# Optimization experiments

Hardware: AMD Instinct MI355X
Metric: run time of the kernel (lower is better)

## Reference

```python
import jax, jax.numpy as jnp
import numpy as np

D = 1024
H = 16
DK = D // H


def setup_inputs() -> dict:
    key = jax.random.key(0)
    ks = jax.random.split(key, 10)
    B, S = 2, 2048
    scale = 1.0 / np.sqrt(D)
    inp = {
        "x": jax.random.normal(ks[0], (B, S, D), dtype=jnp.float32),
        "mask": jax.random.randint(ks[1], (B, S), 0, 2, dtype=jnp.int32),
        "wq": jax.random.normal(ks[2], (D, D), dtype=jnp.float32) * scale,
        "bq": jnp.zeros((D,), dtype=jnp.float32),
        "wk": jax.random.normal(ks[3], (D, D), dtype=jnp.float32) * scale,
        "bk": jnp.zeros((D,), dtype=jnp.float32),
        "wv": jax.random.normal(ks[4], (D, D), dtype=jnp.float32) * scale,
        "bv": jnp.zeros((D,), dtype=jnp.float32),
        "wo": jax.random.normal(ks[5], (D, D), dtype=jnp.float32) * scale,
        "bo": jnp.zeros((D,), dtype=jnp.float32),
    }
    return inp


def reference(x, mask, wq, bq, wk, bk, wv, bv, wo, bo):
    B, S, _ = x.shape
    # torch Linear: y = x @ W.T + b
    def proj(w, b):
        return (jnp.einsum("bsd,ed->bse", x, w) + b).reshape(B, S, H, DK).transpose(0, 2, 1, 3)  # (B,H,S,dk)

    q = proj(wq, bq)
    k = proj(wk, bk)
    v = proj(wv, bv)

    scores = jnp.einsum("bhqd,bhkd->bhqk", q, k) / jnp.sqrt(jnp.float32(DK))  # (B,H,S,S)
    # original: mask.unsqueeze(1).unsqueeze(3) -> (B,1,S,1), masks along the QUERY axis
    m = mask[:, None, :, None]  # (B,1,S,1)
    scores = jnp.where(m == 0, jnp.float32(-1e9), scores)
    attn = jax.nn.softmax(scores, axis=-1)
    ctx = jnp.einsum("bhqk,bhkd->bhqd", attn, v)  # (B,H,S,dk)
    concat = ctx.transpose(0, 2, 1, 3).reshape(B, S, D)
    return jnp.einsum("bsd,ed->bse", concat, wo) + bo
```

## Files before the change

### kernel.cpp

```cpp
#include <hip/hip_runtime.h>
#include <hip/hip_bf16.h>

#define SEQ 2048
#define DM  1024

typedef __attribute__((ext_vector_type(8))) _Float16 f16x8;
typedef __attribute__((ext_vector_type(4)))  float   f32x4;

#define EXP2F(x) __builtin_amdgcn_exp2f(x)

__device__ __forceinline__ ushort f2h(float x) {
    union { _Float16 h; ushort u; } c; c.h = (_Float16)x; return c.u;
}
__device__ __forceinline__ unsigned pk2h(float a, float b) {
    typedef __fp16 fp16v2 __attribute__((ext_vector_type(2)));
    union { fp16v2 h; unsigned u; } c;
    c.h = __builtin_amdgcn_cvt_pkrtz(a, b);
    return c.u;
}

__device__ __forceinline__ void gload16(const void* g, void* l) {
    __builtin_amdgcn_global_load_lds(
        (const __attribute__((address_space(1))) unsigned*)(uintptr_t)g,
        (__attribute__((address_space(3))) unsigned*)(uintptr_t)l, 16, 0, 0);
}

__global__ __launch_bounds__(256)
void cvt_all(const float* __restrict__ x,  const float* __restrict__ wq,
             const float* __restrict__ wk, const float* __restrict__ wv,
             const float* __restrict__ wo,
             ushort* __restrict__ xH, ushort* __restrict__ wH)
{
    const int NX4 = (2 * SEQ * DM) / 4;
    const int NW4 = (DM * DM) / 4;
    const int total = NX4 + 4 * NW4;
    for (int i = blockIdx.x * 256 + threadIdx.x; i < total; i += gridDim.x * 256) {
        float4 v; ushort4* dst;
        if (i < NX4) {
            v = ((const float4*)x)[i];
            dst = (ushort4*)xH + i;
        } else {
            const int j = i - NX4;
            const int wi = j >> 18;
            const int jo = j & (NW4 - 1);
            const float* ws_ = (wi == 0) ? wq : (wi == 1) ? wk : (wi == 2) ? wv : wo;
            v = ((const float4*)ws_)[jo];
            dst = (ushort4*)wH + j;
        }
        ushort4 h;
        h.x = f2h(v.x); h.y = f2h(v.y); h.z = f2h(v.z); h.w = f2h(v.w);
        *dst = h;
    }
}

template<int BM, int BN, int WM, int WN, int MODE>
__global__ __launch_bounds__(WM * WN * 64)
void gemm5(const ushort* __restrict__ A, const ushort* __restrict__ B,
           const float* __restrict__ b0, const float* __restrict__ b1,
           const float* __restrict__ b2,
           ushort* __restrict__ QH, ushort* __restrict__ KH,
           ushort* __restrict__ VH, float* __restrict__ outf, int nmt)
{
    constexpr int NW  = WM * WN;
    constexpr int PR  = BM / WM, PC = BN / WN;
    constexpr int MR  = PR / 16, NR = PC / 16, MH = MR / 2;
    constexpr int APW = (BM / 8) / NW;
    constexpr int BPW = (BN / 8) / NW;
    constexpr int NT  = DM / 64;

    __shared__ ushort A_lds[2][BM * 64];
    __shared__ ushort B_lds[2][BN * 64];

    const int tid = threadIdx.x, w = tid >> 6, lane = tid & 63;
    const int nwg = gridDim.x, q8 = nwg >> 3;
    const int wg  = (blockIdx.x & 7) * q8 + (blockIdx.x >> 3);
    const int m0  = (wg % nmt) * BM, n0 = (wg / nmt) * BN;
    const int wm  = w / WN, wn = w % WN;

    auto stage = [&](int buf, int kt) {
        const int k0 = kt * 64;
#pragma unroll
        for (int j = 0; j < APW; ++j) {
            const int s   = w * APW + j;
            const int row = s * 8 + (lane >> 3);
            const int cl  = (lane & 7) ^ (row & 7);
            gload16(A + (size_t)(m0 + row) * DM + k0 + cl * 8,
                    &A_lds[buf][s * 512]);
        }
#pragma unroll
        for (int j = 0; j < BPW; ++j) {
            const int s   = w * BPW + j;
            const int row = s * 8 + (lane >> 3);
            const int cl  = (lane & 7) ^ (row & 7);
            gload16(B + (size_t)(n0 + row) * DM + k0 + cl * 8,
                    &B_lds[buf][s * 512]);
        }
    };

    f32x4 acc[MR][NR];
#pragma unroll
    for (int i = 0; i < MR; ++i)
#pragma unroll
        for (int j = 0; j < NR; ++j) acc[i][j] = f32x4{0.f, 0.f, 0.f, 0.f};

    stage(0, 0);
    stage(1, 1);

    for (int t = 0; t < NT; ++t) {
        const int buf = t & 1;
        if (t == NT - 1) asm volatile("s_waitcnt vmcnt(0)" ::: "memory");
        else             asm volatile("s_waitcnt vmcnt(8)" ::: "memory");
        __builtin_amdgcn_sched_barrier(0);
        __builtin_amdgcn_s_barrier();

        f16x8 bf_[NR][2];
#pragma unroll
        for (int nf = 0; nf < NR; ++nf) {
            const int r = wn * PC + nf * 16 + (lane & 15);
#pragma unroll
            for (int kb = 0; kb < 2; ++kb) {
                const int c = kb * 4 + (lane >> 4);
                bf_[nf][kb] = *(const f16x8*)&B_lds[buf][r * 64 + ((c ^ (r & 7)) << 3)];
            }
        }
#pragma unroll
        for (int qm = 0; qm < 2; ++qm) {
            f16x8 af_[MH][2];
#pragma unroll
            for (int mf = 0; mf < MH; ++mf) {
                const int r = wm * PR + qm * (PR / 2) + mf * 16 + (lane & 15);
#pragma unroll
                for (int kb = 0; kb < 2; ++kb) {
                    const int c = kb * 4 + (lane >> 4);
                    af_[mf][kb] = *(const f16x8*)&A_lds[buf][r * 64 + ((c ^ (r & 7)) << 3)];
                }
            }
            __builtin_amdgcn_s_setprio(1);
#pragma unroll
            for (int kb = 0; kb < 2; ++kb)
#pragma unroll
                for (int mf = 0; mf < MH; ++mf)
#pragma unroll
                    for (int nf = 0; nf < NR; ++nf)
                        acc[qm * MH + mf][nf] = __builtin_amdgcn_mfma_f32_16x16x32_f16(
                            af_[mf][kb], bf_[nf][kb], acc[qm * MH + mf][nf], 0, 0, 0);
            __builtin_amdgcn_s_setprio(0);
        }
        __builtin_amdgcn_sched_barrier(0);
        __builtin_amdgcn_s_barrier();
        __builtin_amdgcn_sched_barrier(0);
        if (t + 2 < NT) stage(buf, t + 2);
    }

#pragma unroll
    for (int mf = 0; mf < MR; ++mf)
#pragma unroll
        for (int nf = 0; nf < NR; ++nf) {
            const int col  = n0 + wn * PC + nf * 16 + (lane & 15);
            const int row0 = m0 + wm * PR + mf * 16 + ((lane >> 4) << 2);
            f32x4 v = acc[mf][nf];
            if constexpr (MODE == 1) {
                float4 o;
                o.x = v[0] + b0[row0 + 0];
                o.y = v[1] + b0[row0 + 1];
                o.z = v[2] + b0[row0 + 2];
                o.w = v[3] + b0[row0 + 3];
                *(float4*)&outf[(size_t)col * DM + row0] = o;
            } else {
                const int sel = row0 >> 10;
                const int e = row0 & 1023;
                const int b = col >> 11, s = col & 2047;
                const int h = e >> 6, dk = e & 63;
                const float* bp = (sel == 0) ? b0 : (sel == 1) ? b1 : b2;
                const float sc = (sel == 0) ? 0.125f * 1.44269504089f : 1.0f;
                const float v0 = (v[0] + bp[e + 0]) * sc;
                const float v1 = (v[1] + bp[e + 1]) * sc;
                const float v2 = (v[2] + bp[e + 2]) * sc;
                const float v3 = (v[3] + bp[e + 3]) * sc;
                const int bh = b * 16 + h;
                ushort4 hv;
                hv.x = f2h(v0); hv.y = f2h(v1); hv.z = f2h(v2); hv.w = f2h(v3);
                if (sel == 0) {
                    const size_t off = ((size_t)bh * SEQ + s) * 64 + dk;
                    *(ushort4*)&QH[off] = hv;
                } else if (sel == 1) {
                    const size_t off = ((size_t)bh * SEQ + s) * 64 + dk;
                    *(ushort4*)&KH[off] = hv;
                } else {
                    const size_t o0 = ((size_t)bh * 64 + dk) * SEQ + s;
                    VH[o0]           = hv.x;
                    VH[o0 + SEQ]     = hv.y;
                    VH[o0 + 2 * SEQ] = hv.z;
                    VH[o0 + 3 * SEQ] = hv.w;
                }
            }
        }
}

__global__ __launch_bounds__(512, 2)
void attn_k(const ushort* __restrict__ QH, const ushort* __restrict__ KH,
            const ushort* __restrict__ VH, const int* __restrict__ mask,
            ushort* __restrict__ ch)
{
    __shared__ ushort Ks[4][64 * 64];
    __shared__ ushort Vs[4][64 * 64];
    __shared__ ushort Ps[8][16 * 64];

    const int t = threadIdx.x, w = t >> 6, lane = t & 63;
    const int wg = (blockIdx.x & 7) * 64 + (blockIdx.x >> 3);
    const int bh = wg >> 4, qt = wg & 15;
    const int b = bh >> 4, h = bh & 15;
    const int q0 = qt * 128 + w * 16;
    const size_t base = (size_t)bh * SEQ * 64;
    const int lq = lane & 15, cb = lane >> 4;

    const int msk = mask[b * SEQ + q0 + lq];
    f16x8 qf[2];
#pragma unroll
    for (int kb = 0; kb < 2; ++kb) {
        qf[kb] = *(const f16x8*)&QH[base + (size_t)(q0 + lq) * 64 + kb * 32 + cb * 8];
        if (msk == 0) qf[kb] = f16x8{0, 0, 0, 0, 0, 0, 0, 0};
    }

    float l_part = 0.f;
    f32x4 acc[4];
#pragma unroll
    for (int df = 0; df < 4; ++df) acc[df] = f32x4{0.f, 0.f, 0.f, 0.f};

    const int srow = w * 8 + (lane >> 3);
    const int scl  = (lane & 7) ^ (srow & 7);
    const ushort* gK = &KH[base + (size_t)srow * 64 + scl * 8];
    const ushort* gV = &VH[base + (size_t)srow * SEQ + scl * 8];
    const int wbase = w * 512;
    auto issue_pair = [&](const int B0, const int B1) {
        gload16(gK, &Ks[B0][wbase]); gK += 4096;
        gload16(gV, &Vs[B0][wbase]); gV += 64;
        gload16(gK, &Ks[B1][wbase]); gK += 4096;
        gload16(gV, &Vs[B1][wbase]); gV += 64;
    };

    issue_pair(0, 1);
    issue_pair(2, 3);

    auto compute = [&](const int BUF) {
        f32x4 st[4];
#pragma unroll
        for (int mf = 0; mf < 4; ++mf) st[mf] = f32x4{0.f, 0.f, 0.f, 0.f};
        __builtin_amdgcn_s_setprio(1);
#pragma unroll
        for (int mf = 0; mf < 4; ++mf) {
            const int r = mf * 16 + lq;
#pragma unroll
            for (int kb = 0; kb < 2; ++kb) {
                const int p = (kb * 4 + cb) ^ (r & 7);
                f16x8 kf = *(const f16x8*)&Ks[BUF][r * 64 + p * 8];
                st[mf] = __builtin_amdgcn_mfma_f32_16x16x32_f16(kf, qf[kb], st[mf], 0, 0, 0);
            }
        }
        __builtin_amdgcn_s_setprio(0);

#pragma unroll
        for (int mf = 0; mf < 2; ++mf) {
            const float e0 = EXP2F(st[mf][0]);
            const float e1 = EXP2F(st[mf][1]);
            const float e2 = EXP2F(st[mf][2]);
            const float e3 = EXP2F(st[mf][3]);
            l_part += (e0 + e1) + (e2 + e3);
            uint2 pw;
            pw.x = pk2h(e0, e1);
            pw.y = pk2h(e2, e3);
            const int key0 = mf * 16 + (cb << 2);
            const int p = (key0 >> 3) ^ (lq & 7);
            *(uint2*)&Ps[w][lq * 64 + p * 8 + (key0 & 7)] = pw;
        }
        {
            const int p0 = cb ^ (lq & 7);
            f16x8 pf0 = *(const f16x8*)&Ps[w][lq * 64 + p0 * 8];
            __builtin_amdgcn_s_setprio(1);
#pragma unroll
            for (int df = 0; df < 4; ++df) {
                const int r = df * 16 + lq;
                const int p = cb ^ (r & 7);
                f16x8 vf = *(const f16x8*)&Vs[BUF][r * 64 + p * 8];
                acc[df] = __builtin_amdgcn_mfma_f32_16x16x32_f16(vf, pf0, acc[df], 0, 0, 0);
            }
            __builtin_amdgcn_s_setprio(0);
        }
#pragma unroll
        for (int mf = 2; mf < 4; ++mf) {
            const float e0 = EXP2F(st[mf][0]);
            const float e1 = EXP2F(st[mf][1]);
            const float e2 = EXP2F(st[mf][2]);
            const float e3 = EXP2F(st[mf][3]);
            l_part += (e0 + e1) + (e2 + e3);
            uint2 pw;
            pw.x = pk2h(e0, e1);
            pw.y = pk2h(e2, e3);
            const int key0 = mf * 16 + (cb << 2);
            const int p = (key0 >> 3) ^ (lq & 7);
            *(uint2*)&Ps[w][lq * 64 + p * 8 + (key0 & 7)] = pw;
        }
        {
            const int p1 = (4 + cb) ^ (lq & 7);
            f16x8 pf1 = *(const f16x8*)&Ps[w][lq * 64 + p1 * 8];
            __builtin_amdgcn_s_setprio(1);
#pragma unroll
            for (int df = 0; df < 4; ++df) {
                const int r = df * 16 + lq;
                const int p = (4 + cb) ^ (r & 7);
                f16x8 vf = *(const f16x8*)&Vs[BUF][r * 64 + p * 8];
                acc[df] = __builtin_amdgcn_mfma_f32_16x16x32_f16(vf, pf1, acc[df], 0, 0, 0);
            }
            __builtin_amdgcn_s_setprio(0);
        }
    };

    auto step = [&](const int PH, const bool ISSUE, const bool LAST) {
        if (LAST) asm volatile("s_waitcnt vmcnt(0)" ::: "memory");
        else      asm volatile("s_waitcnt vmcnt(4)" ::: "memory");
        __builtin_amdgcn_sched_barrier(0);
        __builtin_amdgcn_s_barrier();
        compute(PH ? 2 : 0);
        compute(PH ? 3 : 1);
        if (ISSUE) {
            __builtin_amdgcn_sched_barrier(0);
            asm volatile("s_waitcnt lgkmcnt(0)" ::: "memory");
            __builtin_amdgcn_s_barrier();
            __builtin_amdgcn_sched_barrier(0);
            if (PH) issue_pair(2, 3); else issue_pair(0, 1);
        }
    };

#pragma unroll 1
    for (int i = 0; i < 7; ++i) {
        step(0, true, false);
        step(1, true, false);
    }
    step(0, false, false);
    step(1, false, true);

    {
        float l_tot = l_part;
        l_tot += __shfl_xor(l_tot, 16);
        l_tot += __shfl_xor(l_tot, 32);
        const float inv = 1.0f / l_tot;
        const int s = q0 + lq;
#pragma unroll
        for (int df = 0; df < 4; ++df) {
            const int e0 = h * 64 + df * 16 + (cb << 2);
            ushort4 hv;
            hv.x = f2h(acc[df][0] * inv);
            hv.y = f2h(acc[df][1] * inv);
            hv.z = f2h(acc[df][2] * inv);
            hv.w = f2h(acc[df][3] * inv);
            *(ushort4*)&ch[(size_t)(b * SEQ + s) * DM + e0] = hv;
        }
    }
}

extern "C" void kernel_launch(void* const* d_in, const int* in_sizes, int n_in,
                              void* d_out, int out_size, void* d_ws, size_t ws_size,
                              hipStream_t stream)
{
    const float* x  = (const float*)d_in[0];
    const int* mask = (const int*)d_in[1];
    const float* wq = (const float*)d_in[2];
    const float* bq = (const float*)d_in[3];
    const float* wk = (const float*)d_in[4];
    const float* bk = (const float*)d_in[5];
    const float* wv = (const float*)d_in[6];
    const float* bv = (const float*)d_in[7];
    const float* wo = (const float*)d_in[8];
    const float* bo = (const float*)d_in[9];
    float* out = (float*)d_out;

    const size_t M1 = 1024 * 1024;
    ushort* W = (ushort*)d_ws;
    ushort* xH = W;
    ushort* wH = W + 4 * M1;
    ushort* QH = W + 8 * M1;
    ushort* KH = W + 12 * M1;
    ushort* VH = W + 16 * M1;

    cvt_all<<<2048, 256, 0, stream>>>(x, wq, wk, wv, wo, xH, wH);

    gemm5<384, 128, 4, 2, 0><<<256, 512, 0, stream>>>(
        wH, xH, bq, bk, bv, QH, KH, VH, nullptr, 8);

    attn_k<<<512, 512, 0, stream>>>(QH, KH, VH, mask, xH);

    gemm5<128, 128, 2, 2, 1><<<256, 256, 0, stream>>>(
        wH + 3 * M1, xH, bo, nullptr, nullptr,
        nullptr, nullptr, nullptr, out, 8);
}
```

Before: 103.4 us.

## Switch attention to 32x32x16 MFMA with 4 waves of 32 queries each

Rewrites the attention kernel to use 32x32x16 f16 MFMA tiles instead of 16x16x32, giving each wave 32 query rows and launching 256-thread blocks (4 waves) rather than 512. K/V tile loads are restructured so each wave loads two row-groups per tile, and the vmcnt wait threshold is adjusted accordingly. The larger MFMA tile is meant to improve operand reuse and reduce LDS reads per FLOP, but it raises register pressure and halves the wave count per block, which may hurt latency hiding.

```diff
diff --git a/kernel.cpp b/kernel.cpp
--- a/kernel.cpp
+++ b/kernel.cpp
@@ -4,8 +4,9 @@
 #define SEQ 2048
 #define DM  1024
 
-typedef __attribute__((ext_vector_type(8))) _Float16 f16x8;
-typedef __attribute__((ext_vector_type(4)))  float   f32x4;
+typedef __attribute__((ext_vector_type(8)))  _Float16 f16x8;
+typedef __attribute__((ext_vector_type(4)))  float    f32x4;
+typedef __attribute__((ext_vector_type(16))) float    f32x16;
 
 #define EXP2F(x) __builtin_amdgcn_exp2f(x)
 
@@ -197,127 +198,113 @@
         }
 }
 
-__global__ __launch_bounds__(512, 2)
+__global__ __launch_bounds__(256, 2)
 void attn_k(const ushort* __restrict__ QH, const ushort* __restrict__ KH,
             const ushort* __restrict__ VH, const int* __restrict__ mask,
             ushort* __restrict__ ch)
 {
     __shared__ ushort Ks[4][64 * 64];
     __shared__ ushort Vs[4][64 * 64];
-    __shared__ ushort Ps[8][16 * 64];
+    __shared__ ushort Ps[4][32 * 64];
 
     const int t = threadIdx.x, w = t >> 6, lane = t & 63;
     const int wg = (blockIdx.x & 7) * 64 + (blockIdx.x >> 3);
     const int bh = wg >> 4, qt = wg & 15;
     const int b = bh >> 4, h = bh & 15;
-    const int q0 = qt * 128 + w * 16;
+    const int q0 = qt * 128 + w * 32;
     const size_t base = (size_t)bh * SEQ * 64;
-    const int lq = lane & 15, cb = lane >> 4;
+    const int lq = lane & 31;
+    const int hi = lane >> 5;
 
     const int msk = mask[b * SEQ + q0 + lq];
-    f16x8 qf[2];
-#pragma unroll
-    for (int kb = 0; kb < 2; ++kb) {
-        qf[kb] = *(const f16x8*)&QH[base + (size_t)(q0 + lq) * 64 + kb * 32 + cb * 8];
+    f16x8 qf[4];
+#pragma unroll
+    for (int kb = 0; kb < 4; ++kb) {
+        qf[kb] = *(const f16x8*)&QH[base + (size_t)(q0 + lq) * 64 + kb * 16 + hi * 8];
         if (msk == 0) qf[kb] = f16x8{0, 0, 0, 0, 0, 0, 0, 0};
     }
 
     float l_part = 0.f;
-    f32x4 acc[4];
-#pragma unroll
-    for (int df = 0; df < 4; ++df) acc[df] = f32x4{0.f, 0.f, 0.f, 0.f};
+    f32x16 acc[2];
+#pragma unroll
+    for (int mf = 0; mf < 2; ++mf)
+#pragma unroll
+        for (int r = 0; r < 16; ++r) acc[mf][r] = 0.f;
 
     const int srow = w * 8 + (lane >> 3);
     const int scl  = (lane & 7) ^ (srow & 7);
-    const ushort* gK = &KH[base + (size_t)srow * 64 + scl * 8];
-    const ushort* gV = &VH[base + (size_t)srow * SEQ + scl * 8];
-    const int wbase = w * 512;
-    auto issue_pair = [&](const int B0, const int B1) {
-        gload16(gK, &Ks[B0][wbase]); gK += 4096;
-        gload16(gV, &Vs[B0][wbase]); gV += 64;
-        gload16(gK, &Ks[B1][wbase]); gK += 4096;
-        gload16(gV, &Vs[B1][wbase]); gV += 64;
-    };
-
-    issue_pair(0, 1);
-    issue_pair(2, 3);
-
-    auto compute = [&](const int BUF) {
-        f32x4 st[4];
-#pragma unroll
-        for (int mf = 0; mf < 4; ++mf) st[mf] = f32x4{0.f, 0.f, 0.f, 0.f};
-        __builtin_amdgcn_s_setprio(1);
-#pragma unroll
-        for (int mf = 0; mf < 4; ++mf) {
-            const int r = mf * 16 + lq;
-#pragma unroll
-            for (int kb = 0; kb < 2; ++kb) {
-                const int p = (kb * 4 + cb) ^ (r & 7);
-                f16x8 kf = *(const f16x8*)&Ks[BUF][r * 64 + p * 8];
-                st[mf] = __builtin_amdgcn_mfma_f32_16x16x32_f16(kf, qf[kb], st[mf], 0, 0, 0);
-            }
-        }
-        __builtin_amdgcn_s_setprio(0);
-
-#pragma unroll
-        for (int mf = 0; mf < 2; ++mf) {
-            const float e0 = EXP2F(st[mf][0]);
-            const float e1 = EXP2F(st[mf][1]);
-            const float e2 = EXP2F(st[mf][2]);
-            const float e3 = EXP2F(st[mf][3]);
+    const ushort* gK0 = &KH[base + (size_t)srow * 64 + scl * 8];
+    const ushort* gK1 = &KH[base + (size_t)(srow + 32) * 64 + scl * 8];
+    const ushort* gV0 = &VH[base + (size_t)srow * SEQ + scl * 8];
+    const ushort* gV1 = &VH[base + (size_t)(srow + 32) * SEQ + scl * 8];
+    const int wb0 = w * 512, wb1 = 2048 + w * 512;
+    auto issue_tile = [&](const int B0) {
+        gload16(gK0, &Ks[B0][wb0]); gK0 += 4096;
+        gload16(gK1, &Ks[B0][wb1]); gK1 += 4096;
+        gload16(gV0, &Vs[B0][wb0]); gV0 += 64;
+        gload16(gV1, &Vs[B0][wb1]); gV1 += 64;
+    };
+
+    issue_tile(0); issue_tile(1);
+    issue_tile(2); issue_tile(3);
+
+    auto sm_half = [&](const f32x16& stv, const int mf) {
+#pragma unroll
+        for (int r4 = 0; r4 < 4; ++r4) {
+            const float e0 = EXP2F(stv[r4 * 4 + 0]);
+            const float e1 = EXP2F(stv[r4 * 4 + 1]);
+            const float e2 = EXP2F(stv[r4 * 4 + 2]);
+            const float e3 = EXP2F(stv[r4 * 4 + 3]);
             l_part += (e0 + e1) + (e2 + e3);
             uint2 pw;
             pw.x = pk2h(e0, e1);
             pw.y = pk2h(e2, e3);
-            const int key0 = mf * 16 + (cb << 2);
-            const int p = (key0 >> 3) ^ (lq & 7);
-            *(uint2*)&Ps[w][lq * 64 + p * 8 + (key0 & 7)] = pw;
-        }
-        {
-            const int p0 = cb ^ (lq & 7);
-            f16x8 pf0 = *(const f16x8*)&Ps[w][lq * 64 + p0 * 8];
-            __builtin_amdgcn_s_setprio(1);
-#pragma unroll
-            for (int df = 0; df < 4; ++df) {
-                const int r = df * 16 + lq;
-                const int p = cb ^ (r & 7);
-                f16x8 vf = *(const f16x8*)&Vs[BUF][r * 64 + p * 8];
-                acc[df] = __builtin_amdgcn_mfma_f32_16x16x32_f16(vf, pf0, acc[df], 0, 0, 0);
-            }
-            __builtin_amdgcn_s_setprio(0);
-        }
-#pragma unroll
-        for (int mf = 2; mf < 4; ++mf) {
-            const float e0 = EXP2F(st[mf][0]);
-            const float e1 = EXP2F(st[mf][1]);
-            const float e2 = EXP2F(st[mf][2]);
-            const float e3 = EXP2F(st[mf][3]);
-            l_part += (e0 + e1) + (e2 + e3);
-            uint2 pw;
-            pw.x = pk2h(e0, e1);
-            pw.y = pk2h(e2, e3);
-            const int key0 = mf * 16 + (cb << 2);
-            const int p = (key0 >> 3) ^ (lq & 7);
-            *(uint2*)&Ps[w][lq * 64 + p * 8 + (key0 & 7)] = pw;
-        }
-        {
-            const int p1 = (4 + cb) ^ (lq & 7);
-            f16x8 pf1 = *(const f16x8*)&Ps[w][lq * 64 + p1 * 8];
-            __builtin_amdgcn_s_setprio(1);
-#pragma unroll
-            for (int df = 0; df < 4; ++df) {
-                const int r = df * 16 + lq;
-                const int p = (4 + cb) ^ (r & 7);
-                f16x8 vf = *(const f16x8*)&Vs[BUF][r * 64 + p * 8];
-                acc[df] = __builtin_amdgcn_mfma_f32_16x16x32_f16(vf, pf1, acc[df], 0, 0, 0);
-            }
-            __builtin_amdgcn_s_setprio(0);
-        }
+            const int p = (r4 + 4 * mf) ^ (lq & 7);
+            *(uint2*)&Ps[w][lq * 64 + p * 8 + 4 * hi] = pw;
+        }
+    };
+    auto pv_slice = [&](const int BUF, const int ks) {
+        const int pc = (ks * 2 + hi) ^ (lq & 7);
+        f16x8 pf = *(const f16x8*)&Ps[w][lq * 64 + pc * 8];
+        __builtin_amdgcn_s_setprio(1);
+#pragma unroll
+        for (int mf2 = 0; mf2 < 2; ++mf2) {
+            f16x8 vf = *(const f16x8*)&Vs[BUF][(mf2 * 32 + lq) * 64 + pc * 8];
+            acc[mf2] = __builtin_amdgcn_mfma_f32_32x32x16_f16(vf, pf, acc[mf2], 0, 0, 0);
+        }
+        __builtin_amdgcn_s_setprio(0);
+    };
+
+    auto compute = [&](const int BUF) {
+        f32x16 st[2];
+#pragma unroll
+        for (int mf = 0; mf < 2; ++mf)
+#pragma unroll
+            for (int r = 0; r < 16; ++r) st[mf][r] = 0.f;
+        __builtin_amdgcn_s_setprio(1);
+#pragma unroll
+        for (int mf = 0; mf < 2; ++mf) {
+            const int rb = (mf * 32 + lq) * 64;
+#pragma unroll
+            for (int kb = 0; kb < 4; ++kb) {
+                const int p = (kb * 2 + hi) ^ (lq & 7);
+                f16x8 kf = *(const f16x8*)&Ks[BUF][rb + p * 8];
+                st[mf] = __builtin_amdgcn_mfma_f32_32x32x16_f16(kf, qf[kb], st[mf], 0, 0, 0);
+            }
+        }
+        __builtin_amdgcn_s_setprio(0);
+
+        sm_half(st[0], 0);
+        pv_slice(BUF, 0);
+        pv_slice(BUF, 1);
+        sm_half(st[1], 1);
+        pv_slice(BUF, 2);
+        pv_slice(BUF, 3);
     };
 
     auto step = [&](const int PH, const bool ISSUE, const bool LAST) {
         if (LAST) asm volatile("s_waitcnt vmcnt(0)" ::: "memory");
-        else      asm volatile("s_waitcnt vmcnt(4)" ::: "memory");
+        else      asm volatile("s_waitcnt vmcnt(8)" ::: "memory");
         __builtin_amdgcn_sched_barrier(0);
         __builtin_amdgcn_s_barrier();
         compute(PH ? 2 : 0);
@@ -327,7 +314,8 @@
             asm volatile("s_waitcnt lgkmcnt(0)" ::: "memory");
             __builtin_amdgcn_s_barrier();
             __builtin_amdgcn_sched_barrier(0);
-            if (PH) issue_pair(2, 3); else issue_pair(0, 1);
+            if (PH) { issue_tile(2); issue_tile(3); }
+            else    { issue_tile(0); issue_tile(1); }
         }
     };
 
@@ -340,21 +328,21 @@
     step(1, false, true);
 
     {
-        float l_tot = l_part;
-        l_tot += __shfl_xor(l_tot, 16);
-        l_tot += __shfl_xor(l_tot, 32);
+        float l_tot = l_part + __shfl_xor(l_part, 32);
         const float inv = 1.0f / l_tot;
         const int s = q0 + lq;
 #pragma unroll
-        for (int df = 0; df < 4; ++df) {
-            const int e0 = h * 64 + df * 16 + (cb << 2);
-            ushort4 hv;
-            hv.x = f2h(acc[df][0] * inv);
-            hv.y = f2h(acc[df][1] * inv);
-            hv.z = f2h(acc[df][2] * inv);
-            hv.w = f2h(acc[df][3] * inv);
-            *(ushort4*)&ch[(size_t)(b * SEQ + s) * DM + e0] = hv;
-        }
+        for (int mf2 = 0; mf2 < 2; ++mf2)
+#pragma unroll
+            for (int r4 = 0; r4 < 4; ++r4) {
+                const int e0 = h * 64 + mf2 * 32 + r4 * 8 + 4 * hi;
+                ushort4 hv;
+                hv.x = f2h(acc[mf2][r4 * 4 + 0] * inv);
+                hv.y = f2h(acc[mf2][r4 * 4 + 1] * inv);
+                hv.z = f2h(acc[mf2][r4 * 4 + 2] * inv);
+                hv.w = f2h(acc[mf2][r4 * 4 + 3] * inv);
+                *(ushort4*)&ch[(size_t)(b * SEQ + s) * DM + e0] = hv;
+            }
     }
 }
 
@@ -387,7 +375,7 @@
     gemm5<384, 128, 4, 2, 0><<<256, 512, 0, stream>>>(
         wH, xH, bq, bk, bv, QH, KH, VH, nullptr, 8);
 
-    attn_k<<<512, 512, 0, stream>>>(QH, KH, VH, mask, xH);
+    attn_k<<<512, 256, 0, stream>>>(QH, KH, VH, mask, xH);
 
     gemm5<128, 128, 2, 2, 1><<<256, 256, 0, stream>>>(
         wH + 3 * M1, xH, bo, nullptr, nullptr,
```

New measurement: 106.0 us. +2.4%, slower.
